# Kernel tuning notes

Hardware: AMD Instinct MI355X
Metric: run time of the kernel (lower is better)

The kernel has to match this reference:

```python
import jax, jax.numpy as jnp
import numpy as np

D_M, L_OBS, ALPHA, D_H = 1024, 2048, 8192, 2048


def setup_inputs() -> dict:
    key = jax.random.key(0)
    k1, k2, k3, k4, k5 = jax.random.split(key, 5)
    x_ts = jax.random.normal(k1, (D_M, L_OBS), dtype=jnp.float32)
    t_ts = jax.random.randint(k2, (D_M, L_OBS), 0, ALPHA, dtype=jnp.int32)
    global_means = jax.random.normal(k3, (D_M,), dtype=jnp.float32)
    W = jax.random.normal(k4, (D_H, D_M), dtype=jnp.float32) * 0.02
    b = jax.random.normal(k5, (D_H,), dtype=jnp.float32) * 0.02
    return {"x_ts": x_ts, "t_ts": t_ts, "global_means": global_means, "W": W, "b": b}


def reference(x_ts, t_ts, global_means, W, b):
    d_m, l_obs = x_ts.shape
    alpha = ALPHA
    # valid observations: non-NaN value and time index within [0, alpha)
    valid = (~jnp.isnan(x_ts)) & (t_ts >= 0) & (t_ts < alpha)
    # route invalid observations to a dummy column `alpha` (dropped afterwards)
    idx = jnp.where(valid, t_ts, alpha)                      # [d_m, l_obs]
    rows = jnp.arange(d_m)[:, None]
    xs = jnp.where(valid, x_ts, 0.0)
    grid_val = jnp.zeros((d_m, alpha + 1), x_ts.dtype).at[rows, idx].set(xs)[:, :alpha]
    grid_ok = jnp.zeros((d_m, alpha + 1), bool).at[rows, idx].set(valid)[:, :alpha]
    # forward-fill: last valid index via cummax, init with global mean
    pos = jnp.arange(alpha)[None, :]                         # [1, alpha]
    last = jax.lax.cummax(jnp.where(grid_ok, pos, -1), axis=1)  # [d_m, alpha]
    filled = jnp.take_along_axis(grid_val, jnp.maximum(last, 0), axis=1)
    regular = jnp.where(last >= 0, filled, global_means[:, None])  # [d_m, alpha]
    # 1x1 conv over time == GEMM over feature dim; output [alpha, d_h]
    return jnp.einsum('ma,hm->ah', regular, W) + b[None, :]
```

## Files before the change

kernel.cpp:

```cpp
#include <hip/hip_runtime.h>
#include <stdint.h>

#define D_M   1024
#define L_OBS 2048
#define ALPHA 8192
#define D_H   2048

typedef __attribute__((ext_vector_type(8))) short short8;
typedef __attribute__((ext_vector_type(4))) float f32x4;

__device__ inline unsigned short f2bf(float f) {
  union { float f; unsigned u; } c; c.f = f;
  unsigned u = c.u;
  u += 0x7fffu + ((u >> 16) & 1u);
  return (unsigned short)(u >> 16);
}

__global__ __launch_bounds__(512) void impute_fill(
    const float* __restrict__ x_ts, const int* __restrict__ t_ts,
    const float* __restrict__ gmean, unsigned short* __restrict__ dst,
    int transposed_out) {
  __shared__ unsigned pack[ALPHA];
  __shared__ float s_wv[8];
  __shared__ int   s_wh[8];

  const int m    = blockIdx.x;
  const int tid  = threadIdx.x;
  const int lane = tid & 63;
  const int wv   = tid >> 6;

  #pragma unroll
  for (int i = 0; i < 4; ++i)
    *reinterpret_cast<uint4*>(&pack[tid * 16 + i * 4]) = make_uint4(0u, 0u, 0u, 0u);
  __syncthreads();

  #pragma unroll
  for (int j = 0; j < 4; ++j) {
    const int l = tid + j * 512;
    const float xv = x_ts[(size_t)m * L_OBS + l];
    const int   tv = t_ts[(size_t)m * L_OBS + l];
    if ((xv == xv) && (tv >= 0) && (tv < ALPHA))
      atomicMax(&pack[tv], ((unsigned)(l + 1) << 16) | (unsigned)f2bf(xv));
  }
  __syncthreads();

  const int base = tid * 16;
  int has = 0; float lv = 0.f;
  #pragma unroll
  for (int i = 0; i < 16; ++i) {
    const unsigned p = pack[base + i];
    if (p >> 16) { has = 1; lv = __uint_as_float(p << 16); }
  }

  int ihas = has; float ilv = lv;
  #pragma unroll
  for (int d = 1; d < 64; d <<= 1) {
    const float pv = __shfl_up(ilv, d, 64);
    const int   ph = __shfl_up(ihas, d, 64);
    if (lane >= d && !ihas) { ihas = ph; ilv = pv; }
  }
  if (lane == 63) { s_wh[wv] = ihas; s_wv[wv] = ilv; }
  __syncthreads();
  if (wv == 0 && lane < 8) {
    int h2 = s_wh[lane]; float v2 = s_wv[lane];
    #pragma unroll
    for (int d = 1; d < 8; d <<= 1) {
      const float pv = __shfl_up(v2, d, 8);
      const int   ph = __shfl_up(h2, d, 8);
      if (lane >= d && !h2) { h2 = ph; v2 = pv; }
    }
    s_wh[lane] = h2; s_wv[lane] = v2;
  }
  __syncthreads();

  const float xlv = __shfl_up(ilv, 1, 64);
  const int   xh_ = __shfl_up(ihas, 1, 64);
  const int   xhas = (lane > 0) ? xh_ : 0;
  float running;
  if (xhas)                         running = xlv;
  else if (wv > 0 && s_wh[wv - 1])  running = s_wv[wv - 1];
  else                              running = gmean[m];

  if (transposed_out) {
    #pragma unroll
    for (int i = 0; i < 16; ++i) {
      const unsigned p = pack[base + i];
      if (p >> 16) running = __uint_as_float(p << 16);
      dst[(size_t)(base + i) * D_M + m] = f2bf(running);
    }
  } else {
    short8 ov0, ov1;
    #pragma unroll
    for (int i = 0; i < 8; ++i) {
      const unsigned p = pack[base + i];
      if (p >> 16) running = __uint_as_float(p << 16);
      ov0[i] = (short)f2bf(running);
    }
    #pragma unroll
    for (int i = 8; i < 16; ++i) {
      const unsigned p = pack[base + i];
      if (p >> 16) running = __uint_as_float(p << 16);
      ov1[i - 8] = (short)f2bf(running);
    }
    *(short8*)&dst[(size_t)m * ALPHA + base]     = ov0;
    *(short8*)&dst[(size_t)m * ALPHA + base + 8] = ov1;
  }
}

__global__ __launch_bounds__(256) void prep(
    const unsigned short* __restrict__ reg, unsigned short* __restrict__ regT,
    const float* __restrict__ W, unsigned short* __restrict__ Wb) {
  __shared__ unsigned short tile[64 * 64];
  const int t = threadIdx.x;

  if (blockIdx.x >= 2048) {
    const int i = ((blockIdx.x - 2048) * 256 + t) * 4;
    const float4 w = *reinterpret_cast<const float4*>(&W[i]);
    ushort4 o;
    o.x = f2bf(w.x); o.y = f2bf(w.y); o.z = f2bf(w.z); o.w = f2bf(w.w);
    *reinterpret_cast<ushort4*>(&Wb[i]) = o;
    return;
  }

  const int m0 = (blockIdx.x & 15) * 64;
  const int A0 = (blockIdx.x >> 4) * 64;

  #pragma unroll
  for (int i = 0; i < 2; ++i) {
    const int m  = i * 32 + (t >> 3);
    const int ao = (t & 7) * 8;
    short8 v = *(const short8*)&reg[(size_t)(m0 + m) * ALPHA + A0 + ao];
    const int s = ((m & 7) ^ (m >> 3)) << 3;
    *(short8*)&tile[m * 64 + (ao ^ s)] = v;
  }
  __syncthreads();
  #pragma unroll
  for (int i = 0; i < 2; ++i) {
    const int a  = i * 32 + (t >> 3);
    const int mo = (t & 7) * 8;
    short8 ov;
    #pragma unroll
    for (int j = 0; j < 8; ++j) {
      const int mm = mo + j;
      const int s  = ((mm & 7) ^ (mm >> 3)) << 3;
      ov[j] = (short)tile[mm * 64 + (a ^ s)];
    }
    *(short8*)&regT[(size_t)(A0 + a) * D_M + m0 + mo] = ov;
  }
}

__global__ __launch_bounds__(256) void wconv(const float* __restrict__ W,
                                             unsigned short* __restrict__ Wb) {
  const int i = (blockIdx.x * 256 + threadIdx.x) * 4;
  const float4 w = *reinterpret_cast<const float4*>(&W[i]);
  ushort4 o;
  o.x = f2bf(w.x); o.y = f2bf(w.y); o.z = f2bf(w.z); o.w = f2bf(w.w);
  *reinterpret_cast<ushort4*>(&Wb[i]) = o;
}

#define GNT3 32

__device__ inline void gload_lds16(const void* g, void* l) {
  __builtin_amdgcn_global_load_lds(
      (const __attribute__((address_space(1))) unsigned int*)g,
      (__attribute__((address_space(3))) unsigned int*)l, 16, 0, 0);
}

#define BARX() { asm volatile("" ::: "memory"); __builtin_amdgcn_s_barrier(); \
                 asm volatile("" ::: "memory"); }

__global__ __launch_bounds__(512, 4) void gemm_bias(
    const unsigned short* __restrict__ A,
    const unsigned short* __restrict__ B,
    const float* __restrict__ bias, float* __restrict__ out) {
  __shared__ char lds[73728];

  const int tid  = threadIdx.x;
  const int lane = tid & 63;
  const int wid  = tid >> 6;
  const int wm   = wid >> 2;
  const int wn   = wid & 3;
  const int xcd  = blockIdx.x & 7;
  const int pos  = blockIdx.x >> 3;
  const int bm   = xcd * 8 + (pos >> 3);
  const int bn   = pos & 7;
  const int a0r = bm * 128, h0 = bn * 256;

  f32x4 acc[4][4] = {};
  short8 af[4], bf[4];

  const int r0 = tid >> 2, s0 = tid & 3;
  const int swzB = (s0 ^ ((r0 >> 1) & 3)) * 16;
  const char* Asrc  = (const char*)A + ((size_t)(a0r + r0) * D_M) * 2 + swzB;
  const char* Bsrc0 = (const char*)B + ((size_t)(h0 + r0) * D_M) * 2 + swzB;
  const char* Bsrc1 = Bsrc0 + (size_t)128 * D_M * 2;

#define STAGE(S, kt) { \
  gload_lds16(Asrc  + (size_t)(kt) * 64, lds + (S) * 8192 + tid * 16); \
  char* bd_ = lds + 24576 + (S) * 16384 + tid * 16; \
  gload_lds16(Bsrc0 + (size_t)(kt) * 64, bd_); \
  gload_lds16(Bsrc1 + (size_t)(kt) * 64, bd_ + 8192); }

  const int rl  = lane & 15;
  const int rsw = (((lane >> 4) ^ ((rl >> 1) & 3))) * 16;
  const int Aro = (wm * 64 + rl) * 64 + rsw;
  const int Bro = 24576 + (wn * 64 + rl) * 64 + rsw;

#define TILE(S, SST, T) { \
  if ((T) < GNT3 - 2) STAGE(SST, (T) + 2); \
  _Pragma("unroll") \
  for (int mf = 0; mf < 4; ++mf) \
    af[mf] = *(const short8*)(lds + (S) * 8192 + Aro + mf * 1024); \
  _Pragma("unroll") \
  for (int nf = 0; nf < 4; ++nf) \
    bf[nf] = *(const short8*)(lds + (S) * 16384 + Bro + nf * 1024); \
  __builtin_amdgcn_s_setprio(1); \
  _Pragma("unroll") \
  for (int mf = 0; mf < 4; ++mf) \
    _Pragma("unroll") \
    for (int nf = 0; nf < 4; ++nf) \
      acc[mf][nf] = __builtin_amdgcn_mfma_f32_16x16x32_bf16(af[mf], bf[nf], acc[mf][nf], 0, 0, 0); \
  __builtin_amdgcn_s_setprio(0); \
  if ((T) < GNT3 - 2)       { asm volatile("s_waitcnt vmcnt(3)" ::: "memory"); } \
  else if ((T) == GNT3 - 2) { asm volatile("s_waitcnt vmcnt(0)" ::: "memory"); } \
  if ((T) < GNT3 - 1) BARX(); }

  STAGE(0, 0); STAGE(1, 1);
  asm volatile("s_waitcnt vmcnt(3)" ::: "memory");
  BARX();

  for (int tt = 0; tt < GNT3 - 2; tt += 3) {
    TILE(0, 2, tt);
    TILE(1, 0, tt + 1);
    TILE(2, 1, tt + 2);
  }
  TILE(0, 2, 30);
  TILE(1, 0, 31);

  const int cl = lane & 15, rq = lane >> 4;
  #pragma unroll
  for (int nf = 0; nf < 4; ++nf) {
    const int h = h0 + wn * 64 + nf * 16 + cl;
    const float bv = bias[h];
    #pragma unroll
    for (int mf = 0; mf < 4; ++mf) {
      const int ar = a0r + wm * 64 + mf * 16 + rq * 4;
      #pragma unroll
      for (int r = 0; r < 4; ++r)
        out[(size_t)(ar + r) * D_H + h] = acc[mf][nf][r] + bv;
    }
  }
#undef STAGE
#undef TILE
}

extern "C" void kernel_launch(void* const* d_in, const int* in_sizes, int n_in,
                              void* d_out, int out_size, void* d_ws, size_t ws_size,
                              hipStream_t stream) {
  const float* x  = (const float*)d_in[0];
  const int*   t  = (const int*)d_in[1];
  const float* gm = (const float*)d_in[2];
  const float* W  = (const float*)d_in[3];
  const float* b  = (const float*)d_in[4];
  float* out = (float*)d_out;

  const size_t SZ_REG = (size_t)ALPHA * D_M * 2;
  const size_t SZ_WB  = (size_t)D_H * D_M * 2;
  const int GRID = (ALPHA / 128) * (D_H / 256);

  if (ws_size >= 2 * SZ_REG + SZ_WB) {
    unsigned short* reg  = (unsigned short*)d_ws;
    unsigned short* regT = (unsigned short*)((char*)d_ws + SZ_REG);
    unsigned short* Wb   = (unsigned short*)((char*)d_ws + 2 * SZ_REG);
    impute_fill<<<D_M, 512, 0, stream>>>(x, t, gm, reg, 0);
    prep<<<4096, 256, 0, stream>>>(reg, regT, W, Wb);
    gemm_bias<<<GRID, 512, 0, stream>>>(regT, Wb, b, out);
  } else {
    unsigned short* regT = (unsigned short*)d_ws;
    unsigned short* Wb   = (unsigned short*)((char*)d_ws + SZ_REG);
    impute_fill<<<D_M, 512, 0, stream>>>(x, t, gm, regT, 1);
    wconv<<<(D_H * D_M) / 1024, 256, 0, stream>>>(W, Wb);
    gemm_bias<<<GRID, 512, 0, stream>>>(regT, Wb, b, out);
  }
}
```

Before: 61.11 us.

## Shrink GEMM tile to 128x128 with K=64 double-buffered stages

Changes the GEMM block tile from 128x256 to 128x128, which doubles the grid to 1024 blocks, and widens each K step to 64 with two pipeline buffers instead of three. Each wave now computes a 64x32 sub-tile in two K halves per stage. The intent is better occupancy and load balance across CUs with fewer barriers per unit of K. The cost is lower operand reuse per block, so global and L2 traffic for A rises. A full vmcnt(0) wait each iteration may also expose load latency.

```diff
diff --git a/kernel.cpp b/kernel.cpp
--- a/kernel.cpp
+++ b/kernel.cpp
@@ -158,7 +158,7 @@
   *reinterpret_cast<ushort4*>(&Wb[i]) = o;
 }
 
-#define GNT3 32
+#define GNT64 16
 
 __device__ inline void gload_lds16(const void* g, void* l) {
   __builtin_amdgcn_global_load_lds(
@@ -173,7 +173,7 @@
     const unsigned short* __restrict__ A,
     const unsigned short* __restrict__ B,
     const float* __restrict__ bias, float* __restrict__ out) {
-  __shared__ char lds[73728];
+  __shared__ char lds[65536];
 
   const int tid  = threadIdx.x;
   const int lane = tid & 63;
@@ -182,65 +182,65 @@
   const int wn   = wid & 3;
   const int xcd  = blockIdx.x & 7;
   const int pos  = blockIdx.x >> 3;
-  const int bm   = xcd * 8 + (pos >> 3);
-  const int bn   = pos & 7;
-  const int a0r = bm * 128, h0 = bn * 256;
-
-  f32x4 acc[4][4] = {};
-  short8 af[4], bf[4];
+  const int bm   = xcd * 8 + (pos >> 4);
+  const int bn   = pos & 15;
+  const int a0r = bm * 128, h0 = bn * 128;
+
+  f32x4 acc[4][2] = {};
+  short8 af[4], bf[2];
 
   const int r0 = tid >> 2, s0 = tid & 3;
   const int swzB = (s0 ^ ((r0 >> 1) & 3)) * 16;
-  const char* Asrc  = (const char*)A + ((size_t)(a0r + r0) * D_M) * 2 + swzB;
-  const char* Bsrc0 = (const char*)B + ((size_t)(h0 + r0) * D_M) * 2 + swzB;
-  const char* Bsrc1 = Bsrc0 + (size_t)128 * D_M * 2;
+  const char* Asrc = (const char*)A + ((size_t)(a0r + r0) * D_M) * 2 + swzB;
+  const char* Bsrc = (const char*)B + ((size_t)(h0 + r0) * D_M) * 2 + swzB;
 
 #define STAGE(S, kt) { \
-  gload_lds16(Asrc  + (size_t)(kt) * 64, lds + (S) * 8192 + tid * 16); \
-  char* bd_ = lds + 24576 + (S) * 16384 + tid * 16; \
-  gload_lds16(Bsrc0 + (size_t)(kt) * 64, bd_); \
-  gload_lds16(Bsrc1 + (size_t)(kt) * 64, bd_ + 8192); }
+  char* a_ = lds + (S) * 32768 + tid * 16; \
+  gload_lds16(Asrc + (size_t)(kt) * 128,      a_); \
+  gload_lds16(Asrc + (size_t)(kt) * 128 + 64, a_ + 8192); \
+  char* b_ = lds + (S) * 32768 + 16384 + tid * 16; \
+  gload_lds16(Bsrc + (size_t)(kt) * 128,      b_); \
+  gload_lds16(Bsrc + (size_t)(kt) * 128 + 64, b_ + 8192); }
 
   const int rl  = lane & 15;
-  const int rsw = (((lane >> 4) ^ ((rl >> 1) & 3))) * 16;
+  const int rsw = ((lane >> 4) ^ ((rl >> 1) & 3)) * 16;
   const int Aro = (wm * 64 + rl) * 64 + rsw;
-  const int Bro = 24576 + (wn * 64 + rl) * 64 + rsw;
-
-#define TILE(S, SST, T) { \
-  if ((T) < GNT3 - 2) STAGE(SST, (T) + 2); \
+  const int Bro = (wn * 32 + rl) * 64 + rsw;
+
+#define HALF(S, H) { \
   _Pragma("unroll") \
   for (int mf = 0; mf < 4; ++mf) \
-    af[mf] = *(const short8*)(lds + (S) * 8192 + Aro + mf * 1024); \
+    af[mf] = *(const short8*)(lds + (S) * 32768 + (H) * 8192 + Aro + mf * 1024); \
   _Pragma("unroll") \
-  for (int nf = 0; nf < 4; ++nf) \
-    bf[nf] = *(const short8*)(lds + (S) * 16384 + Bro + nf * 1024); \
+  for (int nf = 0; nf < 2; ++nf) \
+    bf[nf] = *(const short8*)(lds + (S) * 32768 + 16384 + (H) * 8192 + Bro + nf * 1024); \
   __builtin_amdgcn_s_setprio(1); \
   _Pragma("unroll") \
   for (int mf = 0; mf < 4; ++mf) \
     _Pragma("unroll") \
-    for (int nf = 0; nf < 4; ++nf) \
+    for (int nf = 0; nf < 2; ++nf) \
       acc[mf][nf] = __builtin_amdgcn_mfma_f32_16x16x32_bf16(af[mf], bf[nf], acc[mf][nf], 0, 0, 0); \
-  __builtin_amdgcn_s_setprio(0); \
-  if ((T) < GNT3 - 2)       { asm volatile("s_waitcnt vmcnt(3)" ::: "memory"); } \
-  else if ((T) == GNT3 - 2) { asm volatile("s_waitcnt vmcnt(0)" ::: "memory"); } \
-  if ((T) < GNT3 - 1) BARX(); }
+  __builtin_amdgcn_s_setprio(0); }
+
+#define TILE(S, T) { \
+  if ((T) >= 1 && (T) < GNT64 - 1) STAGE(((T) + 1) & 1, (T) + 1); \
+  HALF(S, 0); \
+  HALF(S, 1); \
+  if ((T) < GNT64 - 1) { asm volatile("s_waitcnt vmcnt(0)" ::: "memory"); BARX(); } }
 
   STAGE(0, 0); STAGE(1, 1);
-  asm volatile("s_waitcnt vmcnt(3)" ::: "memory");
+  asm volatile("s_waitcnt vmcnt(4)" ::: "memory");
   BARX();
 
-  for (int tt = 0; tt < GNT3 - 2; tt += 3) {
-    TILE(0, 2, tt);
-    TILE(1, 0, tt + 1);
-    TILE(2, 1, tt + 2);
-  }
-  TILE(0, 2, 30);
-  TILE(1, 0, 31);
+  for (int tt = 0; tt < GNT64; tt += 2) {
+    TILE(0, tt);
+    TILE(1, tt + 1);
+  }
 
   const int cl = lane & 15, rq = lane >> 4;
   #pragma unroll
-  for (int nf = 0; nf < 4; ++nf) {
-    const int h = h0 + wn * 64 + nf * 16 + cl;
+  for (int nf = 0; nf < 2; ++nf) {
+    const int h = h0 + wn * 32 + nf * 16 + cl;
     const float bv = bias[h];
     #pragma unroll
     for (int mf = 0; mf < 4; ++mf) {
@@ -251,6 +251,7 @@
     }
   }
 #undef STAGE
+#undef HALF
 #undef TILE
 }
 
@@ -266,7 +267,7 @@
 
   const size_t SZ_REG = (size_t)ALPHA * D_M * 2;
   const size_t SZ_WB  = (size_t)D_H * D_M * 2;
-  const int GRID = (ALPHA / 128) * (D_H / 256);
+  const int GRID = (ALPHA / 128) * (D_H / 128);
 
   if (ws_size >= 2 * SZ_REG + SZ_WB) {
     unsigned short* reg  = (unsigned short*)d_ws;
```

Measured after the change: 59.45 us. -2.7%, faster.
